# Kernel optimization log

Hardware: AMD Instinct MI355X
Metric: run time of the kernel (lower is better)

## Reference

```python
import jax, jax.numpy as jnp
import numpy as np

# Convex_f forward. D and mid are fixed tridiagonal matrices:
#   (D x)[i]   = -x[i-1] + 2*x[i] - x[i+1]  for 1 <= i <= n-2, and 0 at i=0, n-1
#   (mid x)[i] = 0.5*(x[i-1] + x[i+1])      for 1 <= i <= n-2,
#                0.5*x[1] at i=0, 0.5*x[n-2] at i=n-1
# We implement these as direct 3-point stencils (same math as the dense matmuls).

B, N, K = 256, 8192, 16

def setup_inputs() -> dict:
    key = jax.random.key(0)
    k1, k2 = jax.random.split(key)
    x = jax.random.normal(k1, (B, N, K), dtype=jnp.float32)
    param = jax.random.normal(k2, (B, N, K), dtype=jnp.float32)
    return {"x": x, "param": param}

def _convex_step(y):
    # y: [B, N, K]
    up, ctr, dn = y[:, :-2], y[:, 1:-1], y[:, 2:]
    Dy_in = -up + 2.0 * ctr - dn                      # interior rows of D @ y
    Dy = jnp.pad(Dy_in, ((0, 0), (1, 1), (0, 0)))     # rows 0 and N-1 zeroed
    mid_y = jnp.concatenate(
        [0.5 * y[:, 1:2], 0.5 * (up + dn), 0.5 * y[:, -2:-1]], axis=1
    )                                                 # mid @ y
    dy = (Dy > 0).astype(y.dtype) * (y - mid_y)
    return y - dy

def reference(x, param):
    y = x + param
    return _convex_step(y) - param
```

## Files before the change

kernel.cpp:

```cpp
#include <hip/hip_runtime.h>


#define B_    256
#define N_    8192
#define K_    16
#define TILE  64
#define KQ    4
#define NTILES (N_ / TILE)

__global__ __launch_bounds__(256)
void convex_kernel(const float4* __restrict__ x4,
                   const float4* __restrict__ p4,
                   float4* __restrict__ o4)
{
    __shared__ float4 ysh[TILE + 2][KQ];

    const int tid = threadIdx.x;
    const int row = tid >> 2;
    const int col = tid & 3;
    const int blk = blockIdx.x;
    const int t   = blk & (NTILES - 1);
    const int b   = blk >> 7;
    const int n0  = t * TILE;

    const long base = ((long)b * N_ + n0) * KQ;
    const long idx  = base + (long)row * KQ + col;

    float4 xv = x4[idx];
    float4 pv = p4[idx];
    float4 yv = make_float4(xv.x + pv.x, xv.y + pv.y, xv.z + pv.z, xv.w + pv.w);
    ysh[row + 1][col] = yv;

    if (tid < 8) {
        const int c = tid & 3;
        float4 h = make_float4(0.f, 0.f, 0.f, 0.f);
        if (tid < 4) {
            if (n0 > 0) {
                float4 hx = x4[base - KQ + c];
                float4 hp = p4[base - KQ + c];
                h = make_float4(hx.x + hp.x, hx.y + hp.y, hx.z + hp.z, hx.w + hp.w);
            }
            ysh[0][c] = h;
        } else {
            if (n0 + TILE < N_) {
                float4 hx = x4[base + (long)TILE * KQ + c];
                float4 hp = p4[base + (long)TILE * KQ + c];
                h = make_float4(hx.x + hp.x, hx.y + hp.y, hx.z + hp.z, hx.w + hp.w);
            }
            ysh[TILE + 1][c] = h;
        }
    }
    __syncthreads();

    const int n = n0 + row;
    float4 r;
    if (n == 0 || n == N_ - 1) {
        r = make_float4(yv.x - pv.x, yv.y - pv.y, yv.z - pv.z, yv.w - pv.w);
    } else {
        float4 a = ysh[row][col];
        float4 d = ysh[row + 2][col];
        float4 m = make_float4(0.5f * (a.x + d.x), 0.5f * (a.y + d.y),
                               0.5f * (a.z + d.z), 0.5f * (a.w + d.w));
        r = make_float4(fminf(yv.x, m.x) - pv.x,
                        fminf(yv.y, m.y) - pv.y,
                        fminf(yv.z, m.z) - pv.z,
                        fminf(yv.w, m.w) - pv.w);
    }
    o4[idx] = r;
}

extern "C" void kernel_launch(void* const* d_in, const int* in_sizes, int n_in,
                              void* d_out, int out_size, void* d_ws, size_t ws_size,
                              hipStream_t stream)
{
    const float4* x = (const float4*)d_in[0];
    const float4* p = (const float4*)d_in[1];
    float4*       o = (float4*)d_out;

    dim3 grid(B_ * NTILES);
    dim3 block(256);
    convex_kernel<<<grid, block, 0, stream>>>(x, p, o);
}
```

Baseline: 299.5 us.

## Register-tile 8 rows per thread with halo loads, drop shared memory, nontemporal stores

Each thread now handles 8 consecutive rows of one float4 column, loading 10 rows (with clamped halos) of x and param into registers. This removes the shared-memory staging and __syncthreads, and cuts the block count by 8x. Output uses nontemporal stores to avoid cache pollution. The exchange is 25% redundant halo loads. Those loads are strided per thread (adjacent lanes differ by 8 rows), which may hurt coalescing.

```diff
diff --git a/kernel.cpp b/kernel.cpp
--- a/kernel.cpp
+++ b/kernel.cpp
@@ -1,83 +1,71 @@
 #include <hip/hip_runtime.h>
 
 
-#define B_    256
-#define N_    8192
-#define K_    16
-#define TILE  64
-#define KQ    4
-#define NTILES (N_ / TILE)
+typedef float f32x4 __attribute__((ext_vector_type(4)));
+
+#define B_      256
+#define N_      8192
+#define KQ      4
+#define R_      8
+#define GROUPS  64
+#define TILE    (GROUPS * R_)
+#define TILES_N (N_ / TILE)
 
 __global__ __launch_bounds__(256)
-void convex_kernel(const float4* __restrict__ x4,
-                   const float4* __restrict__ p4,
-                   float4* __restrict__ o4)
+void convex_kernel(const f32x4* __restrict__ x4,
+                   const f32x4* __restrict__ p4,
+                   f32x4* __restrict__ o4)
 {
-    __shared__ float4 ysh[TILE + 2][KQ];
+    const int tid = threadIdx.x;
+    const int g   = tid >> 2;
+    const int c   = tid & 3;
+    const int t   = blockIdx.x & (TILES_N - 1);
+    const int b   = blockIdx.x >> 4;
+    const int n0  = t * TILE + g * R_;
+    const long rowbase = (long)b * N_;
 
-    const int tid = threadIdx.x;
-    const int row = tid >> 2;
-    const int col = tid & 3;
-    const int blk = blockIdx.x;
-    const int t   = blk & (NTILES - 1);
-    const int b   = blk >> 7;
-    const int n0  = t * TILE;
+    f32x4 xv[R_ + 2], pv[R_ + 2];
+#pragma unroll
+    for (int j = 0; j < R_ + 2; ++j) {
+        int row = n0 - 1 + j;
+        row = row < 0 ? 0 : row;
+        row = row > N_ - 1 ? N_ - 1 : row;
+        const long idx = (rowbase + row) * KQ + c;
+        xv[j] = x4[idx];
+        pv[j] = p4[idx];
+    }
 
-    const long base = ((long)b * N_ + n0) * KQ;
-    const long idx  = base + (long)row * KQ + col;
-
-    float4 xv = x4[idx];
-    float4 pv = p4[idx];
-    float4 yv = make_float4(xv.x + pv.x, xv.y + pv.y, xv.z + pv.z, xv.w + pv.w);
-    ysh[row + 1][col] = yv;
-
-    if (tid < 8) {
-        const int c = tid & 3;
-        float4 h = make_float4(0.f, 0.f, 0.f, 0.f);
-        if (tid < 4) {
-            if (n0 > 0) {
-                float4 hx = x4[base - KQ + c];
-                float4 hp = p4[base - KQ + c];
-                h = make_float4(hx.x + hp.x, hx.y + hp.y, hx.z + hp.z, hx.w + hp.w);
-            }
-            ysh[0][c] = h;
+#pragma unroll
+    for (int j = 0; j < R_; ++j) {
+        const int n = n0 + j;
+        f32x4 r;
+        if (n == 0 || n == N_ - 1) {
+            r = xv[j + 1];
         } else {
-            if (n0 + TILE < N_) {
-                float4 hx = x4[base + (long)TILE * KQ + c];
-                float4 hp = p4[base + (long)TILE * KQ + c];
-                h = make_float4(hx.x + hp.x, hx.y + hp.y, hx.z + hp.z, hx.w + hp.w);
-            }
-            ysh[TILE + 1][c] = h;
+            const f32x4 ym = xv[j]     + pv[j];
+            const f32x4 yc = xv[j + 1] + pv[j + 1];
+            const f32x4 yp = xv[j + 2] + pv[j + 2];
+            const f32x4 m  = 0.5f * (ym + yp);
+            f32x4 mn;
+            mn.x = fminf(yc.x, m.x);
+            mn.y = fminf(yc.y, m.y);
+            mn.z = fminf(yc.z, m.z);
+            mn.w = fminf(yc.w, m.w);
+            r = mn - pv[j + 1];
         }
+        __builtin_nontemporal_store(r, &o4[(rowbase + n) * KQ + c]);
     }
-    __syncthreads();
-
-    const int n = n0 + row;
-    float4 r;
-    if (n == 0 || n == N_ - 1) {
-        r = make_float4(yv.x - pv.x, yv.y - pv.y, yv.z - pv.z, yv.w - pv.w);
-    } else {
-        float4 a = ysh[row][col];
-        float4 d = ysh[row + 2][col];
-        float4 m = make_float4(0.5f * (a.x + d.x), 0.5f * (a.y + d.y),
-                               0.5f * (a.z + d.z), 0.5f * (a.w + d.w));
-        r = make_float4(fminf(yv.x, m.x) - pv.x,
-                        fminf(yv.y, m.y) - pv.y,
-                        fminf(yv.z, m.z) - pv.z,
-                        fminf(yv.w, m.w) - pv.w);
-    }
-    o4[idx] = r;
 }
 
 extern "C" void kernel_launch(void* const* d_in, const int* in_sizes, int n_in,
                               void* d_out, int out_size, void* d_ws, size_t ws_size,
                               hipStream_t stream)
 {
-    const float4* x = (const float4*)d_in[0];
-    const float4* p = (const float4*)d_in[1];
-    float4*       o = (float4*)d_out;
+    const f32x4* x = (const f32x4*)d_in[0];
+    const f32x4* p = (const f32x4*)d_in[1];
+    f32x4*       o = (f32x4*)d_out;
 
-    dim3 grid(B_ * NTILES);
+    dim3 grid(B_ * TILES_N);
     dim3 block(256);
     convex_kernel<<<grid, block, 0, stream>>>(x, p, o);
 }
```

Result: slower. 326.3 us (+9.0%).
